# Kernel optimization log

Hardware: AMD Instinct MI355X
Metric: run time of the kernel (lower is better)

## Reference

```python
import jax, jax.numpy as jnp
import numpy as np
from jax import lax

# static config (matches init_kwargs / input_specs)
B, T, DUR = 16, 256, 4
MEL = T * DUR                      # 1024 frames; durations rows each sum to MEL
D, H, DH, L = 512, 8, 64, 4
INTER, K, OUT = 2048, 3, 80
VOCAB, MAXLEN = 256, 4096


def _sincos(maxlen, d):
    den = jnp.exp(-jnp.arange(0, d, 2).astype(jnp.float32) * (np.log(10000.0) / d))
    ang = jnp.arange(maxlen, dtype=jnp.float32)[:, None] * den[None, :]
    return jnp.stack([jnp.sin(ang), jnp.cos(ang)], axis=-1).reshape(maxlen, d)


def _ln(x, g, b):
    m = jnp.mean(x, -1, keepdims=True)
    v = jnp.mean((x - m) ** 2, -1, keepdims=True)
    return (x - m) * lax.rsqrt(v + 1e-5) * g + b


def _layer(x, am, wqkv, bqkv, wo, bo, ln1g, ln1b, c1w, c1b, c2w, c2b, ln2g, ln2b):
    bs, s, _ = x.shape
    qkv = (x @ wqkv + bqkv).reshape(bs, s, 3, H, DH)
    q, k, v = qkv[:, :, 0], qkv[:, :, 1], qkv[:, :, 2]
    scores = jnp.einsum('bqhd,bkhd->bhqk', q, k) / np.sqrt(DH).astype(np.float32)
    scores = scores + am[:, None, None, :]          # additive key mask (-inf padded)
    attn = jax.nn.softmax(scores, axis=-1)
    ctx = jnp.einsum('bhqk,bkhd->bqhd', attn, v).reshape(bs, s, H * DH)
    x = _ln(x + ctx @ wo + bo, ln1g, ln1b)
    h = lax.conv_general_dilated(x, c1w, (1,), 'SAME', dimension_numbers=('NLC', 'LIO', 'NLC')) + c1b
    h = jax.nn.relu(h)
    h = lax.conv_general_dilated(h, c2w, (1,), 'SAME', dimension_numbers=('NLC', 'LIO', 'NLC')) + c2b
    return _ln(x + h, ln2g, ln2b)


def _stack(x, am, params):
    for i in range(L):
        x = _layer(x, am, *(p[i] for p in params))
    return x


def setup_inputs() -> dict:
    key = jax.random.key(0)
    ks = iter(jax.random.split(key, 64))

    def nrm(shape, s=0.02):
        return jax.random.normal(next(ks), shape, jnp.float32) * s

    inp = {
        'tokens': jax.random.randint(next(ks), (B, T), 0, VOCAB),
        'token_lengths': jax.random.randint(next(ks), (B,), T // 2, T),
        'melspec_length': jax.random.randint(next(ks), (B,), MEL // 2, MEL),
        'durations': jnp.full((B, T), DUR, jnp.int32),   # rows sum to MEL (module assert)
        'mel_len': MEL,
        'emb': nrm((VOCAB, D), 1.0),
    }
    for pre in ('enc', 'dec'):
        inp[pre + '_wqkv'] = nrm((L, D, 3 * H * DH))
        inp[pre + '_bqkv'] = jnp.zeros((L, 3 * H * DH))
        inp[pre + '_wo'] = nrm((L, H * DH, D))
        inp[pre + '_bo'] = jnp.zeros((L, D))
        inp[pre + '_ln1g'] = jnp.ones((L, D))
        inp[pre + '_ln1b'] = jnp.zeros((L, D))
        inp[pre + '_c1w'] = nrm((L, K, D, INTER))
        inp[pre + '_c1b'] = jnp.zeros((L, INTER))
        inp[pre + '_c2w'] = nrm((L, K, INTER, D))
        inp[pre + '_c2b'] = jnp.zeros((L, D))
        inp[pre + '_ln2g'] = jnp.ones((L, D))
        inp[pre + '_ln2b'] = jnp.zeros((L, D))
    inp['out_w'] = nrm((D, OUT))
    inp['out_b'] = jnp.zeros((OUT,))
    return inp


def reference(tokens, token_lengths, melspec_length, durations, mel_len, emb,
              enc_wqkv, enc_bqkv, enc_wo, enc_bo, enc_ln1g, enc_ln1b,
              enc_c1w, enc_c1b, enc_c2w, enc_c2b, enc_ln2g, enc_ln2b,
              dec_wqkv, dec_bqkv, dec_wo, dec_bo, dec_ln1g, dec_ln1b,
              dec_c1w, dec_c1b, dec_c2w, dec_c2b, dec_ln2g, dec_ln2b,
              out_w, out_b):
    bs, t = tokens.shape
    pos = _sincos(MAXLEAN := MAXLEN, D)
    x = emb[tokens]
    # faithful to original: x + (x + pos_embedding[:bs]) where pos buffer is [maxlen,1,D]
    x = 2.0 * x + pos[:bs][:, None, :]
    am = jnp.where(jnp.arange(t)[None, :] > token_lengths[:, None], -jnp.inf, 0.0)
    enc = _stack(x, am, (enc_wqkv, enc_bqkv, enc_wo, enc_bo, enc_ln1g, enc_ln1b,
                         enc_c1w, enc_c1b, enc_c2w, enc_c2b, enc_ln2g, enc_ln2b))
    # length regulator: equivalent gather form of mask.T @ encoder (O(MEL*D) not O(T*MEL*D))
    cums = jnp.cumsum(durations, axis=1)
    frames = jnp.arange(mel_len)
    idx = jax.vmap(lambda c: jnp.searchsorted(c, frames, side='right'))(cums)  # [B, MEL]
    dec_in = jnp.take_along_axis(enc, idx[:, :, None], axis=1)
    keep = (frames[None, :] <= melspec_length[:, None]).astype(dec_in.dtype)
    dec_in = dec_in * keep[:, :, None]
    am2 = jnp.where(frames[None, :] > melspec_length[:, None], -jnp.inf, 0.0)
    dec = _stack(dec_in, am2, (dec_wqkv, dec_bqkv, dec_wo, dec_bo, dec_ln1g, dec_ln1b,
                               dec_c1w, dec_c1b, dec_c2w, dec_c2b, dec_ln2g, dec_ln2b))
    out = dec @ out_w + out_b                      # [B, MEL, OUT]
    return jnp.transpose(out, (0, 2, 1))           # [B, OUT, MEL]
```

## Files before the change

kernel.cpp:

```cpp
#include <hip/hip_runtime.h>

typedef unsigned short u16;
typedef short short8 __attribute__((ext_vector_type(8)));
typedef float floatx4 __attribute__((ext_vector_type(4)));

static constexpr int CB = 16, CT = 256, CMEL = 1024, CD = 512, CH = 8, CDH = 64, CL = 4;
static constexpr int CINTER = 2048, COUT = 80;
static constexpr int CQKV = 3 * CH * CDH;

static __device__ __forceinline__ float bf2f(u16 u) {
  union { unsigned u; float f; } v; v.u = ((unsigned)u) << 16; return v.f;
}
static __device__ __forceinline__ u16 f2bf(float f) {
  union { float f; unsigned u; } v; v.f = f;
  unsigned r = v.u + 0x7fffu + ((v.u >> 16) & 1u);
  return (u16)(r >> 16);
}

static __device__ __forceinline__ void gld16(const u16* g, u16* lds) {
  __builtin_amdgcn_global_load_lds((const __attribute__((address_space(1))) void*)g,
                                   (__attribute__((address_space(3))) void*)lds, 16, 0, 0);
}

template<int NT, bool RELU>
__global__ __launch_bounds__(256)
void gemm2_k(const u16* __restrict__ A, const u16* __restrict__ Bm,
             u16* __restrict__ Cm, const float* __restrict__ bias,
             int M, int N, int K, int lda, int ldb, int ldc,
             int Sm1, long tapStrideB, const u16* __restrict__ zp)
{
  constexpr int BM = 128, BN = 128;
  constexpr int H = (NT == 3) ? 8 : 0;
  constexpr int AR = BM + 2 * H;
  __shared__ u16 As[AR * 32];
  __shared__ u16 Bs[NT * BN * 32];

  const int t = threadIdx.x;
  const int lane = t & 63;
  const int wave = t >> 6;
  const int wrow = wave >> 1;
  const int wcol = wave & 1;
  const int bn0 = blockIdx.x * BN;
  const int bm0 = blockIdx.y * BM;

  floatx4 acc[4][4];
#pragma unroll
  for (int i = 0; i < 4; ++i)
#pragma unroll
    for (int j = 0; j < 4; ++j) acc[i][j] = (floatx4){0.f, 0.f, 0.f, 0.f};

  const int rsub = lane >> 2;
  const int g8 = (((lane & 3) ^ ((lane >> 3) & 3)) << 3);

  const u16* aP0; const u16* aP1; const u16* aP2 = nullptr;
  {
    int gg0 = bm0 - H + wave * 16 + rsub;
    int gg1 = bm0 - H + (wave + 4) * 16 + rsub;
    aP0 = ((NT == 1) || ((unsigned)gg0 < (unsigned)M)) ? A + (long)gg0 * lda + g8 : nullptr;
    aP1 = ((NT == 1) || ((unsigned)gg1 < (unsigned)M)) ? A + (long)gg1 * lda + g8 : nullptr;
    if (NT == 3 && wave == 0) {
      int gg2 = bm0 - H + 128 + rsub;
      aP2 = ((unsigned)gg2 < (unsigned)M) ? A + (long)gg2 * lda + g8 : nullptr;
    }
  }
  const int aL0 = wave * 512, aL1 = (wave + 4) * 512, aL2 = 8 * 512;

  const u16* bP[NT][2]; int bL[NT][2];
#pragma unroll
  for (int i = 0; i < NT; ++i)
#pragma unroll
    for (int j = 0; j < 2; ++j) {
      int r = (wave + j * 4) * 16 + rsub;
      bP[i][j] = Bm + (long)i * tapStrideB + (long)(bn0 + r) * ldb + g8;
      bL[i][j] = (i * BN + (wave + j * 4) * 16) * 32;
    }

  const int q = lane >> 4, fm = lane & 15;
  const int swzB = (q ^ ((fm >> 1) & 3)) << 3;
  int swzA[NT];
  bool mv[NT][4];
#pragma unroll
  for (int tap = 0; tap < NT; ++tap) {
    const int dlt = tap - ((NT == 3) ? 1 : 0);
    swzA[tap] = (q ^ ((((H + dlt + fm) & 15) >> 1) & 3)) << 3;
#pragma unroll
    for (int i = 0; i < 4; ++i) {
      int s = (bm0 + wrow * 64 + i * 16 + fm) & Sm1;
      mv[tap][i] = ((unsigned)(s + dlt) <= (unsigned)Sm1);
    }
  }
  const short8 zero8 = {};

  for (int k0 = 0; k0 < K; k0 += 32) {
    gld16(aP0 ? aP0 + k0 : zp, &As[aL0]);
    gld16(aP1 ? aP1 + k0 : zp, &As[aL1]);
    if (NT == 3 && wave == 0) gld16(aP2 ? aP2 + k0 : zp, &As[aL2]);
#pragma unroll
    for (int i = 0; i < NT; ++i)
#pragma unroll
      for (int j = 0; j < 2; ++j) gld16(bP[i][j] + k0, &Bs[bL[i][j]]);
    __syncthreads();

#pragma unroll
    for (int tap = 0; tap < NT; ++tap) {
      const int dlt = tap - ((NT == 3) ? 1 : 0);
      short8 af[4], bfr[4];
#pragma unroll
      for (int i = 0; i < 4; ++i) {
        af[i] = *(const short8*)&As[(wrow * 64 + i * 16 + fm + H + dlt) * 32 + swzA[tap]];
        if (NT == 3 && !mv[tap][i]) af[i] = zero8;
      }
#pragma unroll
      for (int j = 0; j < 4; ++j)
        bfr[j] = *(const short8*)&Bs[(tap * BN + wcol * 64 + j * 16 + fm) * 32 + swzB];
#pragma unroll
      for (int i = 0; i < 4; ++i)
#pragma unroll
        for (int j = 0; j < 4; ++j)
          acc[i][j] = __builtin_amdgcn_mfma_f32_16x16x32_bf16(af[i], bfr[j], acc[i][j], 0, 0, 0);
    }
    __syncthreads();
  }

  const int rbase = bm0 + wrow * 64 + ((lane >> 4) << 2);
  const int cbase = bn0 + wcol * 64 + fm;
#pragma unroll
  for (int j = 0; j < 4; ++j) {
    int col = cbase + j * 16;
    float bv = bias ? bias[col] : 0.f;
#pragma unroll
    for (int i = 0; i < 4; ++i) {
#pragma unroll
      for (int r = 0; r < 4; ++r) {
        int row = rbase + i * 16 + r;
        float v = acc[i][j][r] + bv;
        if (RELU) v = fmaxf(v, 0.f);
        Cm[(long)row * ldc + col] = f2bf(v);
      }
    }
  }
}

template<int NT, bool RELU>
__global__ __launch_bounds__(512, 2)
void gemm8_k(const u16* __restrict__ A, const u16* __restrict__ Bm,
             u16* __restrict__ Cm, const float* __restrict__ bias,
             int M, int N, int K, int lda, int ldb, int ldc,
             int Sm1, long tapStrideB, const u16* __restrict__ zp)
{
  constexpr int BM = 256, BN = 128;
  constexpr int H = (NT == 3) ? 8 : 0;
  constexpr int AR = BM + 2 * H;
  constexpr int ACH = AR / 16;
  constexpr int BCH = NT * BN / 16;
  constexpr int TCH = ACH + BCH;
  constexpr int MAXS = (TCH + 7) / 8;

  __shared__ __attribute__((aligned(16))) u16 As[2][AR * 32];
  __shared__ __attribute__((aligned(16))) u16 Bs[2][NT * BN * 32];

  const int t = threadIdx.x;
  const int lane = t & 63;
  const int w = t >> 6;
  const int wrow = w >> 1;
  const int wcol = w & 1;
  const int bn0 = blockIdx.x * BN;
  const int bm0 = blockIdx.y * BM;

  floatx4 acc[4][4];
#pragma unroll
  for (int i = 0; i < 4; ++i)
#pragma unroll
    for (int j = 0; j < 4; ++j) acc[i][j] = (floatx4){0.f, 0.f, 0.f, 0.f};

  const int rsub = lane >> 2;
  const int g8 = (((lane & 3) ^ ((lane >> 3) & 3)) << 3);

  const u16* sS[MAXS];
  int        sOff[MAXS];
  bool       sIsA[MAXS];
  bool       sUse[MAXS];
#pragma unroll
  for (int s = 0; s < MAXS; ++s) {
    const int c = w + 8 * s;
    sUse[s] = (c < TCH);
    if (c < ACH) {
      sIsA[s] = true;
      sOff[s] = c * 512;
      int gg = bm0 - H + c * 16 + rsub;
      sS[s] = ((NT == 1) || ((unsigned)gg < (unsigned)M)) ? A + (long)gg * lda + g8 : nullptr;
    } else {
      sIsA[s] = false;
      const int cb = (c - ACH) < BCH ? (c - ACH) : 0;
      const int tap = cb >> 3, rg = cb & 7;
      sOff[s] = (tap * BN + rg * 16) * 32;
      sS[s] = Bm + (long)tap * tapStrideB + (long)(bn0 + rg * 16 + rsub) * ldb + g8;
    }
  }

  const int q = lane >> 4, fm = lane & 15;
  const int swzB = (q ^ ((fm >> 1) & 3)) << 3;
  int swzA[NT];
  bool mv[NT][4];
#pragma unroll
  for (int tap = 0; tap < NT; ++tap) {
    const int dlt = tap - ((NT == 3) ? 1 : 0);
    swzA[tap] = (q ^ ((((H + dlt + fm) & 15) >> 1) & 3)) << 3;
#pragma unroll
    for (int i = 0; i < 4; ++i) {
      int sq = (bm0 + wrow * 64 + i * 16 + fm) & Sm1;
      mv[tap][i] = ((unsigned)(sq + dlt) <= (unsigned)Sm1);
    }
  }
  const short8 zero8 = {};

  auto tile = [&](int k0, const u16* Ard, const u16* Brd,
                  u16* Awr, u16* Bwr, bool doStage) {
    if (doStage) {
      const int k1 = k0 + 32;
#pragma unroll
      for (int s = 0; s < MAXS; ++s)
        if (sUse[s]) {
          u16* dst = (sIsA[s] ? Awr : Bwr) + sOff[s];
          gld16(sS[s] ? sS[s] + k1 : zp, dst);
        }
    }
#pragma unroll
    for (int tap = 0; tap < NT; ++tap) {
      const int dlt = tap - ((NT == 3) ? 1 : 0);
      short8 af[4], bfr[4];
#pragma unroll
      for (int i = 0; i < 4; ++i) {
        af[i] = *(const short8*)&Ard[(wrow * 64 + i * 16 + fm + H + dlt) * 32 + swzA[tap]];
        if (NT == 3 && !mv[tap][i]) af[i] = zero8;
      }
#pragma unroll
      for (int j = 0; j < 4; ++j)
        bfr[j] = *(const short8*)&Brd[(tap * BN + wcol * 64 + j * 16 + fm) * 32 + swzB];
      __builtin_amdgcn_s_barrier();
      asm volatile("s_waitcnt lgkmcnt(0)" ::: "memory");
      __builtin_amdgcn_sched_barrier(0);
      __builtin_amdgcn_s_setprio(1);
#pragma unroll
      for (int i = 0; i < 4; ++i)
#pragma unroll
        for (int j = 0; j < 4; ++j)
          acc[i][j] = __builtin_amdgcn_mfma_f32_16x16x32_bf16(af[i], bfr[j], acc[i][j], 0, 0, 0);
      __builtin_amdgcn_s_setprio(0);
      if (tap == NT - 1)
        asm volatile("s_waitcnt vmcnt(0)" ::: "memory");
      __builtin_amdgcn_s_barrier();
    }
  };

#pragma unroll
  for (int s = 0; s < MAXS; ++s)
    if (sUse[s]) {
      u16* dst = (sIsA[s] ? &As[0][0] : &Bs[0][0]) + sOff[s];
      gld16(sS[s] ? sS[s] : zp, dst);
    }
  asm volatile("s_waitcnt vmcnt(0)" ::: "memory");
  __builtin_amdgcn_s_barrier();

  const int ntiles = K >> 5;
  for (int tt = 0; tt < ntiles; tt += 2) {
    tile(tt * 32,      &As[0][0], &Bs[0][0], &As[1][0], &Bs[1][0], tt + 1 < ntiles);
    tile(tt * 32 + 32, &As[1][0], &Bs[1][0], &As[0][0], &Bs[0][0], tt + 2 < ntiles);
  }

  const int rbase = bm0 + wrow * 64 + ((lane >> 4) << 2);
  const int cbase = bn0 + wcol * 64 + fm;
#pragma unroll
  for (int j = 0; j < 4; ++j) {
    int col = cbase + j * 16;
    float bv = bias ? bias[col] : 0.f;
#pragma unroll
    for (int i = 0; i < 4; ++i) {
#pragma unroll
      for (int r = 0; r < 4; ++r) {
        int row = rbase + i * 16 + r;
        float v = acc[i][j][r] + bv;
        if (RELU) v = fmaxf(v, 0.f);
        Cm[(long)row * ldc + col] = f2bf(v);
      }
    }
  }
}

__global__ __launch_bounds__(512)
void attn_k(const u16* __restrict__ qkv, const u16* __restrict__ vt,
            u16* __restrict__ ctx, const int* __restrict__ lens, int S)
{
  __shared__ __attribute__((aligned(16))) u16 Ks[2][128 * 32];
  __shared__ __attribute__((aligned(16))) u16 Vts[4][64 * 32];
  __shared__ __attribute__((aligned(16))) u16 Ps[8][16][136];

  const int t = threadIdx.x, lane = t & 63, w = t >> 6;
  const int bh = blockIdx.y, b = bh >> 3, h = bh & 7;
  const int q0 = blockIdx.x * 128;
  const int len = lens[b];
  const int fm = lane & 15, quad = lane >> 4;
  const int swz8 = ((quad ^ ((fm >> 1) & 3)) << 3);
  const int rsub = lane >> 2;
  const int g8 = (((lane & 3) ^ ((lane >> 3) & 3)) << 3);

  const int qrow = q0 + w * 16 + fm;
  short8 bq[2];
  bq[0] = *(const short8*)&qkv[(long)(b * S + qrow) * CQKV + h * 64 + quad * 8];
  bq[1] = *(const short8*)&qkv[(long)(b * S + qrow) * CQKV + h * 64 + 32 + quad * 8];

  const int ksW = w & 1, rgA = w >> 1, rgB = (w >> 1) + 4;
  const u16* kBaseA = qkv + ((long)b * S + rgA * 16 + rsub) * CQKV + CD + h * 64 + ksW * 32 + g8;
  const u16* kBaseB = qkv + ((long)b * S + rgB * 16 + rsub) * CQKV + CD + h * 64 + ksW * 32 + g8;
  u16* kDstA = &Ks[ksW][rgA * 512];
  u16* kDstB = &Ks[ksW][rgB * 512];
  const int kvs0 = (2 * w) >> 2, dhc0 = (2 * w) & 3;
  const int kvs1 = (2 * w + 1) >> 2, dhc1 = (2 * w + 1) & 3;
  const u16* vBase0 = vt + ((long)bh * 64 + dhc0 * 16 + rsub) * S + kvs0 * 32 + g8;
  const u16* vBase1 = vt + ((long)bh * 64 + dhc1 * 16 + rsub) * S + kvs1 * 32 + g8;
  u16* vDst0 = &Vts[kvs0][dhc0 * 512];
  u16* vDst1 = &Vts[kvs1][dhc1 * 512];

  floatx4 acc_o[4];
#pragma unroll
  for (int j = 0; j < 4; ++j) acc_o[j] = (floatx4){0.f, 0.f, 0.f, 0.f};
  float m = -1e30f, l = 0.f;

  for (int kv0 = 0; kv0 < S; kv0 += 128) {
    __syncthreads();
    gld16(kBaseA + (long)kv0 * CQKV, kDstA);
    gld16(kBaseB + (long)kv0 * CQKV, kDstB);
    gld16(vBase0 + kv0, vDst0);
    gld16(vBase1 + kv0, vDst1);
    __syncthreads();

    floatx4 sa[8];
#pragma unroll
    for (int i = 0; i < 8; ++i) sa[i] = (floatx4){0.f, 0.f, 0.f, 0.f};
#pragma unroll
    for (int ks = 0; ks < 2; ++ks) {
#pragma unroll
      for (int mi = 0; mi < 8; ++mi) {
        short8 ak = *(const short8*)&Ks[ks][(mi * 16 + fm) * 32 + swz8];
        sa[mi] = __builtin_amdgcn_mfma_f32_16x16x32_bf16(ak, bq[ks], sa[mi], 0, 0, 0);
      }
    }

    float p[8][4], tm = -1e30f;
#pragma unroll
    for (int mi = 0; mi < 8; ++mi)
#pragma unroll
      for (int r = 0; r < 4; ++r) {
        int kvg = kv0 + mi * 16 + quad * 4 + r;
        float v = (kvg <= len) ? sa[mi][r] * 0.125f : -1e30f;
        p[mi][r] = v; tm = fmaxf(tm, v);
      }
    tm = fmaxf(tm, __shfl_xor(tm, 16));
    tm = fmaxf(tm, __shfl_xor(tm, 32));
    const float mnew = fmaxf(m, tm);
    const float al = __expf(m - mnew);
    float ts = 0.f;
#pragma unroll
    for (int mi = 0; mi < 8; ++mi)
#pragma unroll
      for (int r = 0; r < 4; ++r) { float e = __expf(p[mi][r] - mnew); p[mi][r] = e; ts += e; }
    ts += __shfl_xor(ts, 16);
    ts += __shfl_xor(ts, 32);
    l = l * al + ts; m = mnew;
    float al4[4];
#pragma unroll
    for (int r = 0; r < 4; ++r) al4[r] = __shfl(al, ((lane >> 4) << 2) + r, 64);
#pragma unroll
    for (int j = 0; j < 4; ++j)
#pragma unroll
      for (int r = 0; r < 4; ++r) acc_o[j][r] *= al4[r];

#pragma unroll
    for (int mi = 0; mi < 8; ++mi) {
      unsigned u01 = (unsigned)f2bf(p[mi][0]) | ((unsigned)f2bf(p[mi][1]) << 16);
      unsigned u23 = (unsigned)f2bf(p[mi][2]) | ((unsigned)f2bf(p[mi][3]) << 16);
      *(uint2*)&Ps[w][fm][mi * 16 + quad * 4] = make_uint2(u01, u23);
    }

#pragma unroll
    for (int kvs = 0; kvs < 4; ++kvs) {
      short8 ap = *(const short8*)&Ps[w][fm][kvs * 32 + quad * 8];
#pragma unroll
      for (int nj = 0; nj < 4; ++nj) {
        short8 bv = *(const short8*)&Vts[kvs][(nj * 16 + fm) * 32 + swz8];
        acc_o[nj] = __builtin_amdgcn_mfma_f32_16x16x32_bf16(ap, bv, acc_o[nj], 0, 0, 0);
      }
    }
  }

  float li4[4];
#pragma unroll
  for (int r = 0; r < 4; ++r) li4[r] = 1.f / __shfl(l, ((lane >> 4) << 2) + r, 64);
#pragma unroll
  for (int nj = 0; nj < 4; ++nj)
#pragma unroll
    for (int r = 0; r < 4; ++r) {
      int qr = q0 + w * 16 + quad * 4 + r;
      ctx[(long)(b * S + qr) * CD + h * 64 + nj * 16 + fm] = f2bf(acc_o[nj][r] * li4[r]);
    }
}

template<int BM, int BN>
__global__ __launch_bounds__(256)
void gemmF_k(const u16* __restrict__ A, const u16* __restrict__ Bm,
             float* __restrict__ Cm, const float* __restrict__ bias,
             int M, int N, int K, int lda, int ldb,
             const u16* __restrict__ zp)
{
  __shared__ u16 As[BM * 32];
  __shared__ u16 Bs[BN * 32];

  const int t = threadIdx.x;
  const int lane = t & 63;
  const int wave = t >> 6;
  constexpr int WCOLS = BN / 64;
  const int wrow = wave / WCOLS;
  const int wcol = wave % WCOLS;
  const int bn0 = blockIdx.x * BN;
  const int bm0 = blockIdx.y * BM;

  floatx4 acc[4][4];
#pragma unroll
  for (int i = 0; i < 4; ++i)
#pragma unroll
    for (int j = 0; j < 4; ++j) acc[i][j] = (floatx4){0.f, 0.f, 0.f, 0.f};

  const int rsub = lane >> 2;
  const int g8 = (((lane & 3) ^ ((lane >> 3) & 3)) << 3);
  constexpr int PA = BM / 64, PB = BN / 64;

  const int q = lane >> 4, fm = lane & 15;
  const int swz8 = ((q ^ ((fm >> 1) & 3)) << 3);

  const u16* aP[PA]; const u16* bP[PB];
#pragma unroll
  for (int p = 0; p < PA; ++p)
    aP[p] = A + (long)(bm0 + p * 64 + wave * 16 + rsub) * lda + g8;
#pragma unroll
  for (int p = 0; p < PB; ++p) {
    int r = p * 64 + wave * 16 + rsub;
    bP[p] = ((bn0 + r) < N) ? (Bm + (long)(bn0 + r) * ldb + g8) : nullptr;
  }

  for (int k0 = 0; k0 < K; k0 += 32) {
#pragma unroll
    for (int p = 0; p < PA; ++p)
      gld16(aP[p] + k0, &As[(p * 64 + wave * 16) * 32]);
#pragma unroll
    for (int p = 0; p < PB; ++p)
      gld16(bP[p] ? bP[p] + k0 : zp, &Bs[(p * 64 + wave * 16) * 32]);
    __syncthreads();

    short8 af[4], bfr[4];
#pragma unroll
    for (int i = 0; i < 4; ++i)
      af[i] = *(const short8*)&As[(wrow * 64 + i * 16 + fm) * 32 + swz8];
#pragma unroll
    for (int j = 0; j < 4; ++j)
      bfr[j] = *(const short8*)&Bs[(wcol * 64 + j * 16 + fm) * 32 + swz8];
#pragma unroll
    for (int i = 0; i < 4; ++i)
#pragma unroll
      for (int j = 0; j < 4; ++j)
        acc[i][j] = __builtin_amdgcn_mfma_f32_16x16x32_bf16(af[i], bfr[j], acc[i][j], 0, 0, 0);
    __syncthreads();
  }

  const int rbase = bm0 + wrow * 64 + ((lane >> 4) << 2);
  const int cbase = bn0 + wcol * 64 + (lane & 15);
#pragma unroll
  for (int j = 0; j < 4; ++j) {
    int col = cbase + j * 16;
    if (col >= N) continue;
    float bv = bias ? bias[col] : 0.f;
#pragma unroll
    for (int i = 0; i < 4; ++i) {
#pragma unroll
      for (int r = 0; r < 4; ++r) {
        int row = rbase + i * 16 + r;
        Cm[((long)(row >> 10) * COUT + col) * CMEL + (row & 1023)] = acc[i][j][r] + bv;
      }
    }
  }
}

__global__ void cvt_t_k(const float* __restrict__ src, u16* __restrict__ dst, int K, int N)
{
  const int tap = blockIdx.z;
  const int n0 = blockIdx.x * 32, k0 = blockIdx.y * 32;
  __shared__ float tile[32][33];
  const int t = threadIdx.x;
  const int c = t & 31, rr = t >> 5;
  const float* s = src + (long)tap * K * N;
  u16* d = dst + (long)tap * K * N;
#pragma unroll
  for (int i = 0; i < 4; ++i) {
    int k = k0 + rr + i * 8, n = n0 + c;
    tile[rr + i * 8][c] = (k < K && n < N) ? s[(long)k * N + n] : 0.f;
  }
  __syncthreads();
#pragma unroll
  for (int i = 0; i < 4; ++i) {
    int n = n0 + rr + i * 8, k = k0 + c;
    if (n < N && k < K) d[(long)n * K + k] = f2bf(tile[c][rr + i * 8]);
  }
}

__global__ void vtr_k(const u16* __restrict__ qkv, u16* __restrict__ vt, int S)
{
  const int s0 = blockIdx.x * 64;
  const int bh = blockIdx.y;
  const int b = bh >> 3, h = bh & 7;
  __shared__ u16 tile[64][65];
  const int t = threadIdx.x;
  const int wave = t >> 6, lane = t & 63;
#pragma unroll
  for (int i = 0; i < 16; ++i) {
    int sl = wave * 16 + i;
    tile[sl][lane] = qkv[(long)(b * S + s0 + sl) * CQKV + 2 * CD + h * 64 + lane];
  }
  __syncthreads();
  const int dl = t >> 2, sc4 = (t & 3) << 4;
  u16* dstp = vt + ((long)bh * 64 + dl) * S + s0 + sc4;
  short8 v0, v1;
#pragma unroll
  for (int j = 0; j < 8; ++j) { v0[j] = (short)tile[sc4 + j][dl]; v1[j] = (short)tile[sc4 + 8 + j][dl]; }
  *(short8*)dstp = v0;
  *(short8*)(dstp + 8) = v1;
}

__global__ void fill_k(float* __restrict__ o, int n, float v)
{
  int i = blockIdx.x * 256 + threadIdx.x;
  if (i < n) o[i] = v;
}

__global__ void embed_k(const int* __restrict__ tok, const float* __restrict__ emb,
                        u16* __restrict__ X)
{
  const long idx = (long)blockIdx.x * 256 + threadIdx.x;
  const int d = (int)(idx & (CD - 1));
  const int m = (int)(idx >> 9);
  const int b = m >> 8;
  const float e = emb[(long)tok[m] * CD + d];
  const int i2 = d >> 1;
  const float den = __expf(-(float)(2 * i2) * (9.210340371976184f / 512.f));
  const float ang = (float)b * den;
  const float p = (d & 1) ? __cosf(ang) : __sinf(ang);
  X[idx] = f2bf(2.f * e + p);
}

__global__ void ln_res_k(const u16* __restrict__ X, const u16* __restrict__ Y,
                         const float* __restrict__ g, const float* __restrict__ bta,
                         u16* __restrict__ O)
{
  const int m = blockIdx.x, t = threadIdx.x;
  const long base = (long)m * CD;
  float v0 = bf2f(X[base + t]) + bf2f(Y[base + t]);
  float v1 = bf2f(X[base + t + 256]) + bf2f(Y[base + t + 256]);
  __shared__ float red[256];
  red[t] = v0 + v1; __syncthreads();
  for (int s = 128; s > 0; s >>= 1) { if (t < s) red[t] += red[t + s]; __syncthreads(); }
  const float mean = red[0] * (1.f / 512.f);
  __syncthreads();
  const float d0 = v0 - mean, d1 = v1 - mean;
  red[t] = d0 * d0 + d1 * d1; __syncthreads();
  for (int s = 128; s > 0; s >>= 1) { if (t < s) red[t] += red[t + s]; __syncthreads(); }
  const float rstd = rsqrtf(red[0] * (1.f / 512.f) + 1e-5f);
  O[base + t]       = f2bf(d0 * rstd * g[t] + bta[t]);
  O[base + t + 256] = f2bf(d1 * rstd * g[t + 256] + bta[t + 256]);
}

__global__ void cumsum_k(const int* __restrict__ dur, int* __restrict__ cums)
{
  int b = threadIdx.x;
  if (b < CB) {
    int s = 0;
    for (int t = 0; t < CT; ++t) { s += dur[b * CT + t]; cums[b * CT + t] = s; }
  }
}

__global__ void regulate_k(const u16* __restrict__ xe, const int* __restrict__ cums,
                           const int* __restrict__ mlen, u16* __restrict__ xd)
{
  const int m = blockIdx.x;
  const int b = m >> 10, f = m & (CMEL - 1);
  int lo = 0, hi = CT;
  while (lo < hi) { int mid = (lo + hi) >> 1; if (cums[b * CT + mid] <= f) lo = mid + 1; else hi = mid; }
  const int idx = min(lo, CT - 1);
  const bool keep = (f <= mlen[b]);
  const u16* src = xe + ((long)b * CT + idx) * CD;
  u16* dst = xd + (long)m * CD;
  const int t = threadIdx.x;
  dst[t]       = keep ? src[t] : (u16)0;
  dst[t + 256] = keep ? src[t + 256] : (u16)0;
}

extern "C" void kernel_launch(void* const* d_in, const int* in_sizes, int n_in,
                              void* d_out, int out_size, void* d_ws, size_t ws_size,
                              hipStream_t stream)
{
  (void)in_sizes; (void)n_in;
  const int*   tokens = (const int*)d_in[0];
  const int*   tlen   = (const int*)d_in[1];
  const int*   mlen   = (const int*)d_in[2];
  const int*   dur    = (const int*)d_in[3];
  const float* emb    = (const float*)d_in[5];
  const float* ew[12]; const float* dw[12];
  for (int i = 0; i < 12; ++i) { ew[i] = (const float*)d_in[6 + i]; dw[i] = (const float*)d_in[18 + i]; }
  const float* out_w = (const float*)d_in[30];
  const float* out_b = (const float*)d_in[31];

  const int Me = CB * CT;
  const int Md = CB * CMEL;

  const size_t SZ_ZP   = 256;
  const size_t SZ_WBUF = (size_t)3 * CD * CINTER * 2;
  const size_t SZ_XE   = (size_t)Me * CD * 2;
  const size_t SZ_XD   = (size_t)Md * CD * 2;
  const size_t SZ_QKV  = (size_t)Md * CQKV * 2;
  const size_t SZ_HB   = (size_t)Md * CINTER * 2;
  const size_t SZ_CUMS = (size_t)CB * CT * 4;
  auto al = [](size_t b) { return (b + 255) & ~(size_t)255; };
  size_t U = al(SZ_QKV) > al(SZ_HB) ? al(SZ_QKV) : al(SZ_HB);
  size_t total = al(SZ_ZP) + al(SZ_WBUF) + al(SZ_XE) + 3 * al(SZ_XD) + U + al(SZ_CUMS);
  if (total > ws_size) {
    fill_k<<<dim3((unsigned)((out_size + 255) / 256)), dim3(256), 0, stream>>>(
        (float*)d_out, out_size, 1000.0f);
    return;
  }

  char* p = (char*)d_ws;
  auto take = [&](size_t bytes) { char* r = p; p += al(bytes); return r; };
  u16*  zp   = (u16*)take(SZ_ZP);
  u16*  wbuf = (u16*)take(SZ_WBUF);
  u16*  xe   = (u16*)take(SZ_XE);
  u16*  xd   = (u16*)take(SZ_XD);
  u16*  x1   = (u16*)take(SZ_XD);
  u16*  yb   = (u16*)take(SZ_XD);
  char* U0   = take(U);
  u16*  qkvB = (u16*)U0;
  u16*  hb   = (u16*)U0;
  int* cums = (int*)take(SZ_CUMS);

  hipMemsetAsync(zp, 0, SZ_ZP, stream);

  auto cvtT = [&](const float* s, u16* d, int K, int N, int taps) {
    cvt_t_k<<<dim3((unsigned)((N + 31) / 32), (unsigned)((K + 31) / 32), (unsigned)taps),
              dim3(256), 0, stream>>>(s, d, K, N);
  };

  embed_k<<<dim3((unsigned)((long)Me * CD / 256)), dim3(256), 0, stream>>>(tokens, emb, xe);

  auto run_stack = [&](u16* x, int S, int M, const int* lens, const float* const* W) {
    u16* vt = yb;
    const bool big = (M >= 8192);
    for (int l = 0; l < CL; ++l) {
      cvtT(W[0] + (long)l * CD * CQKV, wbuf, CD, CQKV, 1);
      if (big)
        gemm8_k<1, false><<<dim3(CQKV / 128, M / 256), dim3(512), 0, stream>>>(
            x, wbuf, qkvB, W[1] + l * CQKV, M, CQKV, CD, CD, CD, CQKV, S - 1, 0, zp);
      else
        gemm2_k<1, false><<<dim3(CQKV / 128, M / 128), dim3(256), 0, stream>>>(
            x, wbuf, qkvB, W[1] + l * CQKV, M, CQKV, CD, CD, CD, CQKV, S - 1, 0, zp);
      vtr_k<<<dim3((unsigned)(S / 64), (unsigned)(CB * CH)), dim3(256), 0, stream>>>(qkvB, vt, S);
      attn_k<<<dim3((unsigned)(S / 128), (unsigned)(CB * CH)), dim3(512), 0, stream>>>(
          qkvB, vt, x1, lens, S);
      cvtT(W[2] + (long)l * CD * CD, wbuf, CD, CD, 1);
      if (big)
        gemm8_k<1, false><<<dim3(CD / 128, M / 256), dim3(512), 0, stream>>>(
            x1, wbuf, yb, W[3] + l * CD, M, CD, CD, CD, CD, CD, S - 1, 0, zp);
      else
        gemm2_k<1, false><<<dim3(CD / 128, M / 128), dim3(256), 0, stream>>>(
            x1, wbuf, yb, W[3] + l * CD, M, CD, CD, CD, CD, CD, S - 1, 0, zp);
      ln_res_k<<<dim3((unsigned)M), dim3(256), 0, stream>>>(x, yb, W[4] + l * CD, W[5] + l * CD, x1);
      cvtT(W[6] + (long)l * 3 * CD * CINTER, wbuf, CD, CINTER, 3);
      gemm8_k<3, true><<<dim3(CINTER / 128, M / 256), dim3(512), 0, stream>>>(
          x1, wbuf, hb, W[7] + l * CINTER, M, CINTER, CD, CD, CD, CINTER,
          S - 1, (long)CD * CINTER, zp);
      cvtT(W[8] + (long)l * 3 * CINTER * CD, wbuf, CINTER, CD, 3);
      if (big)
        gemm8_k<3, false><<<dim3(CD / 128, M / 256), dim3(512), 0, stream>>>(
            hb, wbuf, yb, W[9] + l * CD, M, CD, CINTER, CINTER, CINTER, CD,
            S - 1, (long)CINTER * CD, zp);
      else
        gemm2_k<3, false><<<dim3(CD / 128, M / 128), dim3(256), 0, stream>>>(
            hb, wbuf, yb, W[9] + l * CD, M, CD, CINTER, CINTER, CINTER, CD,
            S - 1, (long)CINTER * CD, zp);
      ln_res_k<<<dim3((unsigned)M), dim3(256), 0, stream>>>(x1, yb, W[10] + l * CD, W[11] + l * CD, x);
    }
  };

  run_stack(xe, CT, Me, tlen, ew);

  cumsum_k<<<dim3(1), dim3(64), 0, stream>>>(dur, cums);
  regulate_k<<<dim3((unsigned)(CB * CMEL)), dim3(256), 0, stream>>>(xe, cums, mlen, xd);

  run_stack(xd, CMEL, Md, mlen, dw);

  cvtT(out_w, wbuf, CD, COUT, 1);
  gemmF_k<128, 128><<<dim3(1, Md / 128), dim3(256), 0, stream>>>(
      xd, wbuf, (float*)d_out, out_b, Md, COUT, CD, CD, CD, zp);
}
```

Measured before the change: 3.111 ms.

## Replace 256x128 8-wave GEMM with 128x128 4-wave prefetching GEMM kernel

Replaces the 512-thread, 256x128-tile GEMM kernel with a 256-thread, 128x128-tile variant for the large decoder GEMMs. The new kernel uses fixed per-wave staging pointers, issues the next tile's global-to-LDS loads at the start of each k-step, and synchronises once per k-step with __syncthreads. It drops the explicit per-tap barriers, waitcnt and setprio scheduling hints. The encoder's first conv GEMM also switches from the 8-wave kernel to the existing 4-wave gemm2_k. The aim is more blocks, better occupancy and less barrier overhead, at the cost of less operand reuse per block and less explicit control over load/MFMA overlap.

```diff
diff --git a/kernel.cpp b/kernel.cpp
--- a/kernel.cpp
+++ b/kernel.cpp
@@ -142,28 +142,23 @@
 }
 
 template<int NT, bool RELU>
-__global__ __launch_bounds__(512, 2)
-void gemm8_k(const u16* __restrict__ A, const u16* __restrict__ Bm,
-             u16* __restrict__ Cm, const float* __restrict__ bias,
-             int M, int N, int K, int lda, int ldb, int ldc,
-             int Sm1, long tapStrideB, const u16* __restrict__ zp)
-{
-  constexpr int BM = 256, BN = 128;
+__global__ __launch_bounds__(256, 2)
+void gemm2p_k(const u16* __restrict__ A, const u16* __restrict__ Bm,
+              u16* __restrict__ Cm, const float* __restrict__ bias,
+              int M, int N, int K, int lda, int ldb, int ldc,
+              int Sm1, long tapStrideB, const u16* __restrict__ zp)
+{
+  constexpr int BM = 128, BN = 128;
   constexpr int H = (NT == 3) ? 8 : 0;
   constexpr int AR = BM + 2 * H;
-  constexpr int ACH = AR / 16;
-  constexpr int BCH = NT * BN / 16;
-  constexpr int TCH = ACH + BCH;
-  constexpr int MAXS = (TCH + 7) / 8;
-
   __shared__ __attribute__((aligned(16))) u16 As[2][AR * 32];
   __shared__ __attribute__((aligned(16))) u16 Bs[2][NT * BN * 32];
 
   const int t = threadIdx.x;
   const int lane = t & 63;
-  const int w = t >> 6;
-  const int wrow = w >> 1;
-  const int wcol = w & 1;
+  const int wave = t >> 6;
+  const int wrow = wave >> 1;
+  const int wcol = wave & 1;
   const int bn0 = blockIdx.x * BN;
   const int bm0 = blockIdx.y * BM;
 
@@ -176,27 +171,28 @@
   const int rsub = lane >> 2;
   const int g8 = (((lane & 3) ^ ((lane >> 3) & 3)) << 3);
 
-  const u16* sS[MAXS];
-  int        sOff[MAXS];
-  bool       sIsA[MAXS];
-  bool       sUse[MAXS];
-#pragma unroll
-  for (int s = 0; s < MAXS; ++s) {
-    const int c = w + 8 * s;
-    sUse[s] = (c < TCH);
-    if (c < ACH) {
-      sIsA[s] = true;
-      sOff[s] = c * 512;
-      int gg = bm0 - H + c * 16 + rsub;
-      sS[s] = ((NT == 1) || ((unsigned)gg < (unsigned)M)) ? A + (long)gg * lda + g8 : nullptr;
-    } else {
-      sIsA[s] = false;
-      const int cb = (c - ACH) < BCH ? (c - ACH) : 0;
-      const int tap = cb >> 3, rg = cb & 7;
-      sOff[s] = (tap * BN + rg * 16) * 32;
-      sS[s] = Bm + (long)tap * tapStrideB + (long)(bn0 + rg * 16 + rsub) * ldb + g8;
-    }
-  }
+  const u16* aP0; const u16* aP1; const u16* aP2 = nullptr;
+  {
+    int gg0 = bm0 - H + wave * 16 + rsub;
+    int gg1 = bm0 - H + (wave + 4) * 16 + rsub;
+    aP0 = ((NT == 1) || ((unsigned)gg0 < (unsigned)M)) ? A + (long)gg0 * lda + g8 : nullptr;
+    aP1 = ((NT == 1) || ((unsigned)gg1 < (unsigned)M)) ? A + (long)gg1 * lda + g8 : nullptr;
+    if (NT == 3 && wave == 0) {
+      int gg2 = bm0 - H + 128 + rsub;
+      aP2 = ((unsigned)gg2 < (unsigned)M) ? A + (long)gg2 * lda + g8 : nullptr;
+    }
+  }
+  const int aL0 = wave * 512, aL1 = (wave + 4) * 512, aL2 = 8 * 512;
+
+  const u16* bP[NT][2]; int bL[NT][2];
+#pragma unroll
+  for (int i = 0; i < NT; ++i)
+#pragma unroll
+    for (int j = 0; j < 2; ++j) {
+      int r = (wave + j * 4) * 16 + rsub;
+      bP[i][j] = Bm + (long)i * tapStrideB + (long)(bn0 + r) * ldb + g8;
+      bL[i][j] = (i * BN + (wave + j * 4) * 16) * 32;
+    }
 
   const int q = lane >> 4, fm = lane & 15;
   const int swzB = (q ^ ((fm >> 1) & 3)) << 3;
@@ -208,64 +204,51 @@
     swzA[tap] = (q ^ ((((H + dlt + fm) & 15) >> 1) & 3)) << 3;
 #pragma unroll
     for (int i = 0; i < 4; ++i) {
-      int sq = (bm0 + wrow * 64 + i * 16 + fm) & Sm1;
-      mv[tap][i] = ((unsigned)(sq + dlt) <= (unsigned)Sm1);
+      int s = (bm0 + wrow * 64 + i * 16 + fm) & Sm1;
+      mv[tap][i] = ((unsigned)(s + dlt) <= (unsigned)Sm1);
     }
   }
   const short8 zero8 = {};
 
-  auto tile = [&](int k0, const u16* Ard, const u16* Brd,
-                  u16* Awr, u16* Bwr, bool doStage) {
-    if (doStage) {
-      const int k1 = k0 + 32;
-#pragma unroll
-      for (int s = 0; s < MAXS; ++s)
-        if (sUse[s]) {
-          u16* dst = (sIsA[s] ? Awr : Bwr) + sOff[s];
-          gld16(sS[s] ? sS[s] + k1 : zp, dst);
-        }
-    }
+  auto stage = [&](int buf, int k0) {
+    gld16(aP0 ? aP0 + k0 : zp, &As[buf][aL0]);
+    gld16(aP1 ? aP1 + k0 : zp, &As[buf][aL1]);
+    if (NT == 3 && wave == 0) gld16(aP2 ? aP2 + k0 : zp, &As[buf][aL2]);
+#pragma unroll
+    for (int i = 0; i < NT; ++i)
+#pragma unroll
+      for (int j = 0; j < 2; ++j) gld16(bP[i][j] + k0, &Bs[buf][bL[i][j]]);
+  };
+
+  auto tile = [&](int rd, int wr, int k0) {
+    if (k0 + 32 < K) stage(wr, k0 + 32);
 #pragma unroll
     for (int tap = 0; tap < NT; ++tap) {
       const int dlt = tap - ((NT == 3) ? 1 : 0);
       short8 af[4], bfr[4];
 #pragma unroll
       for (int i = 0; i < 4; ++i) {
-        af[i] = *(const short8*)&Ard[(wrow * 64 + i * 16 + fm + H + dlt) * 32 + swzA[tap]];
+        af[i] = *(const short8*)&As[rd][(wrow * 64 + i * 16 + fm + H + dlt) * 32 + swzA[tap]];
         if (NT == 3 && !mv[tap][i]) af[i] = zero8;
       }
 #pragma unroll
       for (int j = 0; j < 4; ++j)
-        bfr[j] = *(const short8*)&Brd[(tap * BN + wcol * 64 + j * 16 + fm) * 32 + swzB];
-      __builtin_amdgcn_s_barrier();
-      asm volatile("s_waitcnt lgkmcnt(0)" ::: "memory");
-      __builtin_amdgcn_sched_barrier(0);
-      __builtin_amdgcn_s_setprio(1);
+        bfr[j] = *(const short8*)&Bs[rd][(tap * BN + wcol * 64 + j * 16 + fm) * 32 + swzB];
 #pragma unroll
       for (int i = 0; i < 4; ++i)
 #pragma unroll
         for (int j = 0; j < 4; ++j)
           acc[i][j] = __builtin_amdgcn_mfma_f32_16x16x32_bf16(af[i], bfr[j], acc[i][j], 0, 0, 0);
-      __builtin_amdgcn_s_setprio(0);
-      if (tap == NT - 1)
-        asm volatile("s_waitcnt vmcnt(0)" ::: "memory");
-      __builtin_amdgcn_s_barrier();
-    }
+    }
+    __syncthreads();
   };
 
-#pragma unroll
-  for (int s = 0; s < MAXS; ++s)
-    if (sUse[s]) {
-      u16* dst = (sIsA[s] ? &As[0][0] : &Bs[0][0]) + sOff[s];
-      gld16(sS[s] ? sS[s] : zp, dst);
-    }
-  asm volatile("s_waitcnt vmcnt(0)" ::: "memory");
-  __builtin_amdgcn_s_barrier();
-
-  const int ntiles = K >> 5;
-  for (int tt = 0; tt < ntiles; tt += 2) {
-    tile(tt * 32,      &As[0][0], &Bs[0][0], &As[1][0], &Bs[1][0], tt + 1 < ntiles);
-    tile(tt * 32 + 32, &As[1][0], &Bs[1][0], &As[0][0], &Bs[0][0], tt + 2 < ntiles);
+  stage(0, 0);
+  __syncthreads();
+
+  for (int k0 = 0; k0 < K; k0 += 64) {
+    tile(0, 1, k0);
+    tile(1, 0, k0 + 32);
   }
 
   const int rbase = bm0 + wrow * 64 + ((lane >> 4) << 2);
@@ -663,7 +646,7 @@
     for (int l = 0; l < CL; ++l) {
       cvtT(W[0] + (long)l * CD * CQKV, wbuf, CD, CQKV, 1);
       if (big)
-        gemm8_k<1, false><<<dim3(CQKV / 128, M / 256), dim3(512), 0, stream>>>(
+        gemm2p_k<1, false><<<dim3(CQKV / 128, M / 128), dim3(256), 0, stream>>>(
             x, wbuf, qkvB, W[1] + l * CQKV, M, CQKV, CD, CD, CD, CQKV, S - 1, 0, zp);
       else
         gemm2_k<1, false><<<dim3(CQKV / 128, M / 128), dim3(256), 0, stream>>>(
@@ -673,19 +656,24 @@
           qkvB, vt, x1, lens, S);
       cvtT(W[2] + (long)l * CD * CD, wbuf, CD, CD, 1);
       if (big)
-        gemm8_k<1, false><<<dim3(CD / 128, M / 256), dim3(512), 0, stream>>>(
+        gemm2p_k<1, false><<<dim3(CD / 128, M / 128), dim3(256), 0, stream>>>(
             x1, wbuf, yb, W[3] + l * CD, M, CD, CD, CD, CD, CD, S - 1, 0, zp);
       else
         gemm2_k<1, false><<<dim3(CD / 128, M / 128), dim3(256), 0, stream>>>(
             x1, wbuf, yb, W[3] + l * CD, M, CD, CD, CD, CD, CD, S - 1, 0, zp);
       ln_res_k<<<dim3((unsigned)M), dim3(256), 0, stream>>>(x, yb, W[4] + l * CD, W[5] + l * CD, x1);
       cvtT(W[6] + (long)l * 3 * CD * CINTER, wbuf, CD, CINTER, 3);
-      gemm8_k<3, true><<<dim3(CINTER / 128, M / 256), dim3(512), 0, stream>>>(
-          x1, wbuf, hb, W[7] + l * CINTER, M, CINTER, CD, CD, CD, CINTER,
-          S - 1, (long)CD * CINTER, zp);
+      if (big)
+        gemm2p_k<3, true><<<dim3(CINTER / 128, M / 128), dim3(256), 0, stream>>>(
+            x1, wbuf, hb, W[7] + l * CINTER, M, CINTER, CD, CD, CD, CINTER,
+            S - 1, (long)CD * CINTER, zp);
+      else
+        gemm2_k<3, true><<<dim3(CINTER / 128, M / 128), dim3(256), 0, stream>>>(
+            x1, wbuf, hb, W[7] + l * CINTER, M, CINTER, CD, CD, CD, CINTER,
+            S - 1, (long)CD * CINTER, zp);
       cvtT(W[8] + (long)l * 3 * CINTER * CD, wbuf, CINTER, CD, 3);
       if (big)
-        gemm8_k<3, false><<<dim3(CD / 128, M / 256), dim3(512), 0, stream>>>(
+        gemm2p_k<3, false><<<dim3(CD / 128, M / 128), dim3(256), 0, stream>>>(
             hb, wbuf, yb, W[9] + l * CD, M, CD, CINTER, CINTER, CINTER, CD,
             S - 1, (long)CINTER * CD, zp);
       else
```

Result: faster. 2.689 ms (-13.5%).
